# Performance work log

Hardware: AMD Instinct MI355X
Metric: run time of the kernel (lower is better)

The kernel has to match this reference:

```python
import jax, jax.numpy as jnp
import numpy as np
import math

D_MODEL = 1024
NUM_HEADS = 16
HEAD_DIM = D_MODEL // NUM_HEADS  # 64
PLANE_DIM = HEAD_DIM // 2        # 32
ROPE_THETA = 10000.0
ROPE_PERIOD = 1024.0
ROPE_SCALE = 2.0 * math.pi / ROPE_PERIOD


def _inv_freq():
    # 1 / theta^(arange(0, plane_dim, 2)/plane_dim)  -> [plane_dim//2] = [16]
    return 1.0 / ROPE_THETA ** (jnp.arange(0, PLANE_DIM, 2, dtype=jnp.float32) / PLANE_DIM)


def _rotate_pairs(x, sin, cos):
    # x: [B,H,N,P], sin/cos: [B,1,N,P//2]
    x0 = x[..., 0::2]
    x1 = x[..., 1::2]
    y0 = x0 * cos - x1 * sin
    y1 = x0 * sin + x1 * cos
    return jnp.stack([y0, y1], axis=-1).reshape(x.shape)


def _apply_rope_2d(x, pos_2d, inv_freq):
    # x: [B,H,N,D], pos_2d: [B,N,2]
    ang_x = pos_2d[..., 0] * ROPE_SCALE  # [B,N]
    ang_y = pos_2d[..., 1] * ROPE_SCALE
    fx = ang_x[..., None] * inv_freq     # [B,N,P//2]
    fy = ang_y[..., None] * inv_freq
    sin_x, cos_x = jnp.sin(fx)[:, None], jnp.cos(fx)[:, None]  # [B,1,N,P//2]
    sin_y, cos_y = jnp.sin(fy)[:, None], jnp.cos(fy)[:, None]
    xp, yp = x[..., :PLANE_DIM], x[..., PLANE_DIM:]
    xp = _rotate_pairs(xp, sin_x, cos_x)
    yp = _rotate_pairs(yp, sin_y, cos_y)
    return jnp.concatenate([xp, yp], axis=-1)


def setup_inputs() -> dict:
    key = jax.random.key(0)
    ks = jax.random.split(key, 12)
    B, N, d = 2, 2048, D_MODEL
    s = 1.0 / math.sqrt(d)
    return {
        "x": jax.random.normal(ks[0], (B, N, d), jnp.float32),
        "q_positions": jax.random.uniform(ks[1], (B, N, 2), jnp.float32) * ROPE_PERIOD,
        "kv_positions": jax.random.uniform(ks[2], (B, N, 2), jnp.float32) * ROPE_PERIOD,
        "Wq": jax.random.normal(ks[3], (d, d), jnp.float32) * s,
        "bq": jnp.zeros((d,), jnp.float32),
        "Wk": jax.random.normal(ks[4], (d, d), jnp.float32) * s,
        "bk": jnp.zeros((d,), jnp.float32),
        "Wv": jax.random.normal(ks[5], (d, d), jnp.float32) * s,
        "bv": jnp.zeros((d,), jnp.float32),
        "Wo": jax.random.normal(ks[6], (d, d), jnp.float32) * s,
        "bo": jnp.zeros((d,), jnp.float32),
    }


def reference(x, q_positions, kv_positions, Wq, bq, Wk, bk, Wv, bv, Wo, bo):
    B, Nq, _ = x.shape
    H, D = NUM_HEADS, HEAD_DIM
    inv_freq = _inv_freq()
    # fused-style QKV projections (torch Linear: x @ W.T + b)
    q = (jnp.einsum('bnd,od->bno', x, Wq) + bq).reshape(B, Nq, H, D).transpose(0, 2, 1, 3)
    k = (jnp.einsum('bnd,od->bno', x, Wk) + bk).reshape(B, Nq, H, D).transpose(0, 2, 1, 3)
    v = (jnp.einsum('bnd,od->bno', x, Wv) + bv).reshape(B, Nq, H, D).transpose(0, 2, 1, 3)
    q = _apply_rope_2d(q, q_positions, inv_freq)
    k = _apply_rope_2d(k, kv_positions, inv_freq)
    logits = jnp.einsum('bhqd,bhkd->bhqk', q, k) / math.sqrt(D)
    attn = jax.nn.softmax(logits, axis=-1)
    out = jnp.einsum('bhqk,bhkd->bhqd', attn, v)
    out = out.transpose(0, 2, 1, 3).reshape(B, Nq, D_MODEL)
    return jnp.einsum('bnd,od->bno', out, Wo) + bo
```

## Files before the change

### kernel.cpp

```cpp
#include <hip/hip_runtime.h>
#include <math.h>

#define SEQ   2048
#define DM    1024
#define NTOK  4096
#define HEADS 16
#define HDIM  64
#define ROPE_SCALE 0.006135923151542565f

#define TM 64
#define TN 64
#define TK 32

typedef __attribute__((ext_vector_type(8))) short bf16x8;
typedef __attribute__((ext_vector_type(4))) float f32x4;

__device__ __forceinline__ unsigned short f2bf(float f) {
    unsigned int u = __float_as_uint(f);
    return (unsigned short)((u + 0x7FFFu + ((u >> 16) & 1u)) >> 16);
}
__device__ __forceinline__ float bf2f(unsigned short h) {
    return __uint_as_float(((unsigned int)h) << 16);
}

__global__ __launch_bounds__(256) void qkv_rope(
    const float* __restrict__ x,
    const float* __restrict__ Wq, const float* __restrict__ bq,
    const float* __restrict__ Wk, const float* __restrict__ bk,
    const float* __restrict__ Wv, const float* __restrict__ bv,
    const float* __restrict__ qpos, const float* __restrict__ kpos,
    float* __restrict__ qo, float* __restrict__ ko, float* __restrict__ vo)
{
    const int proj = blockIdx.z;
    const float* W   = proj==0 ? Wq : (proj==1 ? Wk : Wv);
    const float* bia = proj==0 ? bq : (proj==1 ? bk : bv);
    float* out       = proj==0 ? qo : (proj==1 ? ko : vo);
    const float* pos = proj==0 ? qpos : kpos;

    __shared__ __align__(16) float As[TK][TM+4];
    __shared__ __align__(16) float Bs[TK][TN+4];

    const int tx = threadIdx.x, ty = threadIdx.y;
    const int tid = ty*16 + tx;
    const int m0 = blockIdx.y * TM;
    const int n0 = blockIdx.x * TN;

    float acc[4][4] = {};

    for (int k0 = 0; k0 < DM; k0 += TK) {
        for (int f = tid; f < 512; f += 256) {
            const int r = f >> 3, c4 = (f & 7) * 4;
            float4 a = *(const float4*)(x + (size_t)(m0 + r)*DM + k0 + c4);
            As[c4+0][r]=a.x; As[c4+1][r]=a.y; As[c4+2][r]=a.z; As[c4+3][r]=a.w;
            float4 b = *(const float4*)(W + (size_t)(n0 + r)*DM + k0 + c4);
            Bs[c4+0][r]=b.x; Bs[c4+1][r]=b.y; Bs[c4+2][r]=b.z; Bs[c4+3][r]=b.w;
        }
        __syncthreads();
        #pragma unroll
        for (int kk = 0; kk < TK; ++kk) {
            float4 a4 = *(const float4*)&As[kk][ty*4];
            float4 b4 = *(const float4*)&Bs[kk][tx*4];
            const float av[4] = {a4.x,a4.y,a4.z,a4.w};
            const float bv4[4] = {b4.x,b4.y,b4.z,b4.w};
            #pragma unroll
            for (int i=0;i<4;++i)
                #pragma unroll
                for (int j=0;j<4;++j)
                    acc[i][j] += av[i]*bv4[j];
        }
        __syncthreads();
    }

    #pragma unroll
    for (int i=0;i<4;++i) {
        const int tok = m0 + ty*4 + i;
        const int b   = tok >> 11;
        const int n   = tok & (SEQ-1);
        if (proj == 2) {
            #pragma unroll
            for (int j=0;j<4;++j) {
                const int o = n0 + tx*4 + j;
                const int h = o >> 6, dd = o & 63;
                out[(((size_t)(b*HEADS + h))*SEQ + n)*HDIM + dd] = acc[i][j] + bia[o];
            }
        } else {
            #pragma unroll
            for (int j=0;j<4;j+=2) {
                const int o = n0 + tx*4 + j;
                const int h = o >> 6, dd = o & 63;
                const int plane = (dd < 32) ? 0 : 1;
                const float p = pos[((size_t)(b*SEQ + n))*2 + plane];
                const float e = (float)(dd & 31) * (1.0f/32.0f);
                const float invf = 1.0f / powf(10000.0f, e);
                const float ang = p * ROPE_SCALE * invf;
                float s, c;
                sincosf(ang, &s, &c);
                const float a0 = acc[i][j]   + bia[o];
                const float a1 = acc[i][j+1] + bia[o+1];
                const size_t base = (((size_t)(b*HEADS + h))*SEQ + n)*HDIM + dd;
                out[base]   = a0*c - a1*s;
                out[base+1] = a0*s + a1*c;
            }
        }
    }
}

#define KB 32

__global__ __launch_bounds__(256) void attn_mfma(
    const float* __restrict__ q, const float* __restrict__ k,
    const float* __restrict__ v, float* __restrict__ ao)
{
    const int bh  = blockIdx.y;
    const int qb0 = blockIdx.x * 128;
    const int tid = threadIdx.x;
    const int lane = tid & 63;
    const int wv   = tid >> 6;
    const int col  = lane & 15;
    const int grp  = lane >> 4;

    __shared__ __align__(16) unsigned short Khi[KB][72];
    __shared__ __align__(16) unsigned short Klo[KB][72];
    __shared__ __align__(16) unsigned short Vthi[HDIM][40];
    __shared__ __align__(16) unsigned short Vtlo[HDIM][40];
    __shared__ __align__(16) unsigned short Pb[4][32][40];

    const float* kbase = k + (size_t)bh*SEQ*HDIM;
    const float* vbase = v + (size_t)bh*SEQ*HDIM;

    bf16x8 qhi[2][2], qlo[2][2];
    #pragma unroll
    for (int mf = 0; mf < 2; ++mf)
        #pragma unroll
        for (int ks = 0; ks < 2; ++ks) {
            const float* p = q + ((size_t)bh*SEQ + qb0 + wv*32 + mf*16 + col)*HDIM
                               + ks*32 + grp*8;
            float4 f0 = ((const float4*)p)[0];
            float4 f1 = ((const float4*)p)[1];
            float fv[8] = {f0.x,f0.y,f0.z,f0.w,f1.x,f1.y,f1.z,f1.w};
            bf16x8 h, l;
            #pragma unroll
            for (int j = 0; j < 8; ++j) {
                unsigned short hb = f2bf(fv[j]);
                h[j] = (short)hb;
                l[j] = (short)f2bf(fv[j] - bf2f(hb));
            }
            qhi[mf][ks] = h; qlo[mf][ks] = l;
        }

    f32x4 o[2][4];
    #pragma unroll
    for (int mf=0; mf<2; ++mf)
        #pragma unroll
        for (int nf=0; nf<4; ++nf)
            o[mf][nf] = (f32x4)0.f;
    float mrun[2][4], lrun[2][4];
    #pragma unroll
    for (int mf=0; mf<2; ++mf)
        #pragma unroll
        for (int r=0; r<4; ++r) { mrun[mf][r] = -INFINITY; lrun[mf][r] = 0.f; }

    for (int kt = 0; kt < SEQ; kt += KB) {
        __syncthreads();
        {
            const int row = tid >> 3, c0 = (tid & 7) * 8;
            const float* src = kbase + (size_t)(kt + row)*HDIM + c0;
            float4 f0 = ((const float4*)src)[0];
            float4 f1 = ((const float4*)src)[1];
            float fv[8] = {f0.x,f0.y,f0.z,f0.w,f1.x,f1.y,f1.z,f1.w};
            bf16x8 h, l;
            #pragma unroll
            for (int j = 0; j < 8; ++j) {
                unsigned short hb = f2bf(fv[j]);
                h[j] = (short)hb;
                l[j] = (short)f2bf(fv[j] - bf2f(hb));
            }
            *(bf16x8*)&Khi[row][c0] = h;
            *(bf16x8*)&Klo[row][c0] = l;
        }
        {
            const int key = tid & 31, db = tid >> 5;
            const float* src = vbase + (size_t)(kt + key)*HDIM + db*8;
            float4 f0 = ((const float4*)src)[0];
            float4 f1 = ((const float4*)src)[1];
            float fv[8] = {f0.x,f0.y,f0.z,f0.w,f1.x,f1.y,f1.z,f1.w};
            #pragma unroll
            for (int j = 0; j < 8; ++j) {
                unsigned short hb = f2bf(fv[j]);
                Vthi[db*8+j][key] = hb;
                Vtlo[db*8+j][key] = f2bf(fv[j] - bf2f(hb));
            }
        }
        __syncthreads();

        f32x4 s[2][2];
        #pragma unroll
        for (int mf=0; mf<2; ++mf)
            #pragma unroll
            for (int nf=0; nf<2; ++nf)
                s[mf][nf] = (f32x4)0.f;
        #pragma unroll
        for (int ks = 0; ks < 2; ++ks) {
            bf16x8 kh[2], kl[2];
            #pragma unroll
            for (int nf = 0; nf < 2; ++nf) {
                kh[nf] = *(const bf16x8*)&Khi[nf*16 + col][ks*32 + grp*8];
                kl[nf] = *(const bf16x8*)&Klo[nf*16 + col][ks*32 + grp*8];
            }
            #pragma unroll
            for (int mf = 0; mf < 2; ++mf)
                #pragma unroll
                for (int nf = 0; nf < 2; ++nf) {
                    s[mf][nf] = __builtin_amdgcn_mfma_f32_16x16x32_bf16(qhi[mf][ks], kh[nf], s[mf][nf], 0,0,0);
                    s[mf][nf] = __builtin_amdgcn_mfma_f32_16x16x32_bf16(qlo[mf][ks], kh[nf], s[mf][nf], 0,0,0);
                    s[mf][nf] = __builtin_amdgcn_mfma_f32_16x16x32_bf16(qhi[mf][ks], kl[nf], s[mf][nf], 0,0,0);
                }
        }

        #pragma unroll
        for (int mf=0; mf<2; ++mf)
            #pragma unroll
            for (int nf=0; nf<2; ++nf)
                s[mf][nf] *= 0.125f;

        #pragma unroll
        for (int mf = 0; mf < 2; ++mf) {
            #pragma unroll
            for (int r = 0; r < 4; ++r) {
                float m2 = fmaxf(s[mf][0][r], s[mf][1][r]);
                m2 = fmaxf(m2, __shfl_xor(m2, 1, 16));
                m2 = fmaxf(m2, __shfl_xor(m2, 2, 16));
                m2 = fmaxf(m2, __shfl_xor(m2, 4, 16));
                m2 = fmaxf(m2, __shfl_xor(m2, 8, 16));
                const float mnew = fmaxf(mrun[mf][r], m2);
                const float corr = __expf(mrun[mf][r] - mnew);
                mrun[mf][r] = mnew;
                const float p0 = __expf(s[mf][0][r] - mnew);
                const float p1 = __expf(s[mf][1][r] - mnew);
                float ts = p0 + p1;
                ts += __shfl_xor(ts, 1, 16);
                ts += __shfl_xor(ts, 2, 16);
                ts += __shfl_xor(ts, 4, 16);
                ts += __shfl_xor(ts, 8, 16);
                lrun[mf][r] = lrun[mf][r]*corr + ts;
                #pragma unroll
                for (int nf=0; nf<4; ++nf) o[mf][nf][r] *= corr;
                Pb[wv][mf*16 + grp*4 + r][col]      = f2bf(p0);
                Pb[wv][mf*16 + grp*4 + r][16 + col] = f2bf(p1);
            }
        }

        bf16x8 pa[2];
        #pragma unroll
        for (int mf=0; mf<2; ++mf)
            pa[mf] = *(const bf16x8*)&Pb[wv][mf*16 + col][grp*8];
        #pragma unroll
        for (int nf = 0; nf < 4; ++nf) {
            bf16x8 vh = *(const bf16x8*)&Vthi[nf*16 + col][grp*8];
            bf16x8 vl = *(const bf16x8*)&Vtlo[nf*16 + col][grp*8];
            #pragma unroll
            for (int mf = 0; mf < 2; ++mf) {
                o[mf][nf] = __builtin_amdgcn_mfma_f32_16x16x32_bf16(pa[mf], vh, o[mf][nf], 0,0,0);
                o[mf][nf] = __builtin_amdgcn_mfma_f32_16x16x32_bf16(pa[mf], vl, o[mf][nf], 0,0,0);
            }
        }
    }

    const int b = bh >> 4, h = bh & 15;
    #pragma unroll
    for (int mf = 0; mf < 2; ++mf)
        #pragma unroll
        for (int r = 0; r < 4; ++r) {
            const float inv = 1.0f / lrun[mf][r];
            const int n = qb0 + wv*32 + mf*16 + grp*4 + r;
            float* orow = ao + (((size_t)b*SEQ + n)*HEADS + h)*HDIM;
            #pragma unroll
            for (int nf = 0; nf < 4; ++nf)
                orow[nf*16 + col] = o[mf][nf][r] * inv;
        }
}

__global__ __launch_bounds__(256) void out_proj(
    const float* __restrict__ ao, const float* __restrict__ Wo,
    const float* __restrict__ bo, float* __restrict__ out)
{
    __shared__ __align__(16) float As[TK][TM+4];
    __shared__ __align__(16) float Bs[TK][TN+4];

    const int tx = threadIdx.x, ty = threadIdx.y;
    const int tid = ty*16 + tx;
    const int m0 = blockIdx.y * TM;
    const int n0 = blockIdx.x * TN;

    float acc[4][4] = {};

    for (int k0 = 0; k0 < DM; k0 += TK) {
        for (int f = tid; f < 512; f += 256) {
            const int r = f >> 3, c4 = (f & 7) * 4;
            float4 a = *(const float4*)(ao + (size_t)(m0 + r)*DM + k0 + c4);
            As[c4+0][r]=a.x; As[c4+1][r]=a.y; As[c4+2][r]=a.z; As[c4+3][r]=a.w;
            float4 b = *(const float4*)(Wo + (size_t)(n0 + r)*DM + k0 + c4);
            Bs[c4+0][r]=b.x; Bs[c4+1][r]=b.y; Bs[c4+2][r]=b.z; Bs[c4+3][r]=b.w;
        }
        __syncthreads();
        #pragma unroll
        for (int kk = 0; kk < TK; ++kk) {
            float4 a4 = *(const float4*)&As[kk][ty*4];
            float4 b4 = *(const float4*)&Bs[kk][tx*4];
            const float av[4] = {a4.x,a4.y,a4.z,a4.w};
            const float bv4[4] = {b4.x,b4.y,b4.z,b4.w};
            #pragma unroll
            for (int i=0;i<4;++i)
                #pragma unroll
                for (int j=0;j<4;++j)
                    acc[i][j] += av[i]*bv4[j];
        }
        __syncthreads();
    }

    #pragma unroll
    for (int i=0;i<4;++i) {
        const int tok = m0 + ty*4 + i;
        #pragma unroll
        for (int j=0;j<4;++j) {
            const int o = n0 + tx*4 + j;
            out[(size_t)tok*DM + o] = acc[i][j] + bo[o];
        }
    }
}

extern "C" void kernel_launch(void* const* d_in, const int* in_sizes, int n_in,
                              void* d_out, int out_size, void* d_ws, size_t ws_size,
                              hipStream_t stream)
{
    const float* x    = (const float*)d_in[0];
    const float* qpos = (const float*)d_in[1];
    const float* kpos = (const float*)d_in[2];
    const float* Wq   = (const float*)d_in[3];
    const float* bq   = (const float*)d_in[4];
    const float* Wk   = (const float*)d_in[5];
    const float* bk   = (const float*)d_in[6];
    const float* Wv   = (const float*)d_in[7];
    const float* bv   = (const float*)d_in[8];
    const float* Wo   = (const float*)d_in[9];
    const float* bo   = (const float*)d_in[10];
    float* out = (float*)d_out;

    float* qw = (float*)d_ws;
    float* kw = qw + (size_t)NTOK*DM;
    float* vw = kw + (size_t)NTOK*DM;
    float* aw = vw + (size_t)NTOK*DM;

    dim3 blk(16,16);
    qkv_rope<<<dim3(DM/TN, NTOK/TM, 3), blk, 0, stream>>>(
        x, Wq,bq, Wk,bk, Wv,bv, qpos,kpos, qw,kw,vw);
    attn_mfma<<<dim3(SEQ/128, 2*HEADS), 256, 0, stream>>>(qw, kw, vw, aw);
    out_proj<<<dim3(DM/TN, NTOK/TM), blk, 0, stream>>>(aw, Wo, bo, out);
}
```

Baseline: 753.2 us.

## Replace FP32 SIMT projection GEMMs with split-bf16 MFMA GEMM using packed swizzled tiles

Result: faster. 657.5 us (-12.7%).

```diff
diff --git a/kernel.cpp b/kernel.cpp
--- a/kernel.cpp
+++ b/kernel.cpp
@@ -7,10 +7,7 @@
 #define HEADS 16
 #define HDIM  64
 #define ROPE_SCALE 0.006135923151542565f
-
-#define TM 64
-#define TN 64
-#define TK 32
+#define L2_10000   13.287712379549449f
 
 typedef __attribute__((ext_vector_type(8))) short bf16x8;
 typedef __attribute__((ext_vector_type(4))) float f32x4;
@@ -23,83 +20,184 @@
     return __uint_as_float(((unsigned int)h) << 16);
 }
 
-__global__ __launch_bounds__(256) void qkv_rope(
-    const float* __restrict__ x,
-    const float* __restrict__ Wq, const float* __restrict__ bq,
-    const float* __restrict__ Wk, const float* __restrict__ bk,
-    const float* __restrict__ Wv, const float* __restrict__ bv,
+__device__ __forceinline__ void split8(const float* __restrict__ src, bf16x8& h, bf16x8& l) {
+    float4 f0 = ((const float4*)src)[0];
+    float4 f1 = ((const float4*)src)[1];
+    float fv[8] = {f0.x,f0.y,f0.z,f0.w,f1.x,f1.y,f1.z,f1.w};
+    #pragma unroll
+    for (int j = 0; j < 8; ++j) {
+        unsigned short hb = f2bf(fv[j]);
+        h[j] = (short)hb;
+        l[j] = (short)f2bf(fv[j] - bf2f(hb));
+    }
+}
+
+__device__ __forceinline__ void gload16(const void* g, void* l) {
+    __builtin_amdgcn_global_load_lds(
+        (const __attribute__((address_space(1))) unsigned int*)g,
+        (__attribute__((address_space(3))) unsigned int*)l, 16, 0, 0);
+}
+
+__global__ __launch_bounds__(256) void pack_swz(
+    const float* __restrict__ src, unsigned short* __restrict__ dst)
+{
+    const int idx = blockIdx.x*256 + threadIdx.x;
+    const int e = idx * 8;
+    const int r = e >> 10, k0 = e & 1023;
+    bf16x8 h, l;
+    split8(src + (size_t)r*DM + k0, h, l);
+    const int mt = r >> 7, rl = r & 127;
+    const int kt = k0 >> 5, kl = k0 & 31;
+    char* tb = (char*)(dst + ((size_t)(mt*32 + kt))*8192);
+    const int sw = (rl & 7) << 4;
+    *(bf16x8*)(tb + ((rl*128 + kl*2) ^ sw))      = h;
+    *(bf16x8*)(tb + ((rl*128 + 64 + kl*2) ^ sw)) = l;
+}
+
+__global__ __launch_bounds__(256) void pack_swz3(
+    const float* __restrict__ Wq, const float* __restrict__ Wk,
+    const float* __restrict__ Wv, unsigned short* __restrict__ dst)
+{
+    const int idx = blockIdx.x*256 + threadIdx.x;
+    const int e = idx * 8;
+    const int r = e >> 10, k0 = e & 1023;
+    const int proj = r >> 10;
+    const float* W = proj==0 ? Wq : (proj==1 ? Wk : Wv);
+    bf16x8 h, l;
+    split8(W + (size_t)(r & 1023)*DM + k0, h, l);
+    const int mt = r >> 7, rl = r & 127;
+    const int kt = k0 >> 5, kl = k0 & 31;
+    char* tb = (char*)(dst + ((size_t)(mt*32 + kt))*8192);
+    const int sw = (rl & 7) << 4;
+    *(bf16x8*)(tb + ((rl*128 + kl*2) ^ sw))      = h;
+    *(bf16x8*)(tb + ((rl*128 + 64 + kl*2) ^ sw)) = l;
+}
+
+__global__ __launch_bounds__(256) void gemm_mfma(
+    const unsigned short* __restrict__ Ap, const unsigned short* __restrict__ Bp,
+    const int mode,
+    const float* __restrict__ bq, const float* __restrict__ bk,
+    const float* __restrict__ bv,
     const float* __restrict__ qpos, const float* __restrict__ kpos,
-    float* __restrict__ qo, float* __restrict__ ko, float* __restrict__ vo)
+    float* __restrict__ qo, float* __restrict__ ko, float* __restrict__ vo,
+    const float* __restrict__ bo, float* __restrict__ outp)
 {
-    const int proj = blockIdx.z;
-    const float* W   = proj==0 ? Wq : (proj==1 ? Wk : Wv);
-    const float* bia = proj==0 ? bq : (proj==1 ? bk : bv);
-    float* out       = proj==0 ? qo : (proj==1 ? ko : vo);
-    const float* pos = proj==0 ? qpos : kpos;
-
-    __shared__ __align__(16) float As[TK][TM+4];
-    __shared__ __align__(16) float Bs[TK][TN+4];
-
-    const int tx = threadIdx.x, ty = threadIdx.y;
-    const int tid = ty*16 + tx;
-    const int m0 = blockIdx.y * TM;
-    const int n0 = blockIdx.x * TN;
-
-    float acc[4][4] = {};
-
-    for (int k0 = 0; k0 < DM; k0 += TK) {
-        for (int f = tid; f < 512; f += 256) {
-            const int r = f >> 3, c4 = (f & 7) * 4;
-            float4 a = *(const float4*)(x + (size_t)(m0 + r)*DM + k0 + c4);
-            As[c4+0][r]=a.x; As[c4+1][r]=a.y; As[c4+2][r]=a.z; As[c4+3][r]=a.w;
-            float4 b = *(const float4*)(W + (size_t)(n0 + r)*DM + k0 + c4);
-            Bs[c4+0][r]=b.x; Bs[c4+1][r]=b.y; Bs[c4+2][r]=b.z; Bs[c4+3][r]=b.w;
-        }
+    __shared__ __align__(16) unsigned short Ab[2][8192];
+    __shared__ __align__(16) unsigned short Bb[2][8192];
+
+    const int tid = threadIdx.x, lane = tid & 63, wv = tid >> 6;
+    const int col = lane & 15, grp = lane >> 4;
+    const int wr = wv >> 1, wc = wv & 1;
+    const int mt = blockIdx.y, nt = blockIdx.x;
+
+    f32x4 acc[4][4];
+    #pragma unroll
+    for (int mf=0; mf<4; ++mf)
+        #pragma unroll
+        for (int nf=0; nf<4; ++nf)
+            acc[mf][nf] = (f32x4)0.f;
+
+    auto stage = [&](int buf, int kt) {
+        const char* ga = (const char*)(Ap + ((size_t)(mt*32 + kt))*8192);
+        const char* gb = (const char*)(Bp + ((size_t)(nt*32 + kt))*8192);
+        char* la = (char*)&Ab[buf][0];
+        char* lb = (char*)&Bb[buf][0];
+        #pragma unroll
+        for (int rep = 0; rep < 4; ++rep) {
+            const int o = wv*4096 + rep*1024;
+            gload16(ga + o + lane*16, la + o);
+            gload16(gb + o + lane*16, lb + o);
+        }
+    };
+
+    stage(0, 0);
+    int cur = 0;
+    for (int kt = 0; kt < 32; ++kt) {
         __syncthreads();
-        #pragma unroll
-        for (int kk = 0; kk < TK; ++kk) {
-            float4 a4 = *(const float4*)&As[kk][ty*4];
-            float4 b4 = *(const float4*)&Bs[kk][tx*4];
-            const float av[4] = {a4.x,a4.y,a4.z,a4.w};
-            const float bv4[4] = {b4.x,b4.y,b4.z,b4.w};
-            #pragma unroll
-            for (int i=0;i<4;++i)
+        if (kt < 31) stage(cur ^ 1, kt + 1);
+        const char* A = (const char*)&Ab[cur][0];
+        const char* B = (const char*)&Bb[cur][0];
+        bf16x8 ah[4], al[4], bh[4], bl[4];
+        #pragma unroll
+        for (int mf = 0; mf < 4; ++mf) {
+            const int rl = wr*64 + mf*16 + col;
+            const int base = rl*128 + grp*16;
+            const int sw = (rl & 7) << 4;
+            ah[mf] = *(const bf16x8*)(A + (base ^ sw));
+            al[mf] = *(const bf16x8*)(A + ((base + 64) ^ sw));
+        }
+        #pragma unroll
+        for (int nf = 0; nf < 4; ++nf) {
+            const int rl = wc*64 + nf*16 + col;
+            const int base = rl*128 + grp*16;
+            const int sw = (rl & 7) << 4;
+            bh[nf] = *(const bf16x8*)(B + (base ^ sw));
+            bl[nf] = *(const bf16x8*)(B + ((base + 64) ^ sw));
+        }
+        #pragma unroll
+        for (int mf = 0; mf < 4; ++mf)
+            #pragma unroll
+            for (int nf = 0; nf < 4; ++nf) {
+                acc[mf][nf] = __builtin_amdgcn_mfma_f32_16x16x32_bf16(ah[mf], bh[nf], acc[mf][nf], 0,0,0);
+                acc[mf][nf] = __builtin_amdgcn_mfma_f32_16x16x32_bf16(ah[mf], bl[nf], acc[mf][nf], 0,0,0);
+                acc[mf][nf] = __builtin_amdgcn_mfma_f32_16x16x32_bf16(al[mf], bh[nf], acc[mf][nf], 0,0,0);
+            }
+        cur ^= 1;
+    }
+
+    const int m0 = mt*128, n0 = nt*128;
+    if (mode == 1) {
+        #pragma unroll
+        for (int nf = 0; nf < 4; ++nf) {
+            const int n = n0 + wc*64 + nf*16 + col;
+            const float bn = bo[n];
+            #pragma unroll
+            for (int mf = 0; mf < 4; ++mf)
                 #pragma unroll
-                for (int j=0;j<4;++j)
-                    acc[i][j] += av[i]*bv4[j];
-        }
-        __syncthreads();
-    }
-
-    #pragma unroll
-    for (int i=0;i<4;++i) {
-        const int tok = m0 + ty*4 + i;
-        const int b   = tok >> 11;
-        const int n   = tok & (SEQ-1);
-        if (proj == 2) {
-            #pragma unroll
-            for (int j=0;j<4;++j) {
-                const int o = n0 + tx*4 + j;
-                const int h = o >> 6, dd = o & 63;
-                out[(((size_t)(b*HEADS + h))*SEQ + n)*HDIM + dd] = acc[i][j] + bia[o];
-            }
-        } else {
-            #pragma unroll
-            for (int j=0;j<4;j+=2) {
-                const int o = n0 + tx*4 + j;
-                const int h = o >> 6, dd = o & 63;
-                const int plane = (dd < 32) ? 0 : 1;
-                const float p = pos[((size_t)(b*SEQ + n))*2 + plane];
-                const float e = (float)(dd & 31) * (1.0f/32.0f);
-                const float invf = 1.0f / powf(10000.0f, e);
-                const float ang = p * ROPE_SCALE * invf;
-                float s, c;
-                sincosf(ang, &s, &c);
-                const float a0 = acc[i][j]   + bia[o];
-                const float a1 = acc[i][j+1] + bia[o+1];
-                const size_t base = (((size_t)(b*HEADS + h))*SEQ + n)*HDIM + dd;
-                out[base]   = a0*c - a1*s;
-                out[base+1] = a0*s + a1*c;
+                for (int i = 0; i < 4; ++i) {
+                    const int tok = m0 + wr*64 + mf*16 + grp*4 + i;
+                    outp[(size_t)tok*DM + n] = acc[mf][nf][i] + bn;
+                }
+        }
+    } else {
+        const int proj = n0 >> 10;
+        const float* bb = proj==0 ? bq : (proj==1 ? bk : bv);
+        float* op       = proj==0 ? qo : (proj==1 ? ko : vo);
+        const float* pp = proj==0 ? qpos : kpos;
+        #pragma unroll
+        for (int nf = 0; nf < 4; ++nf) {
+            const int n  = n0 + wc*64 + nf*16 + col;
+            const int nn = n & 1023;
+            const int h  = nn >> 6, dd = nn & 63;
+            const float bn = bb[nn];
+            if (proj == 2) {
+                #pragma unroll
+                for (int mf = 0; mf < 4; ++mf)
+                    #pragma unroll
+                    for (int i = 0; i < 4; ++i) {
+                        const int tok = m0 + wr*64 + mf*16 + grp*4 + i;
+                        const int b = tok >> 11, sq = tok & 2047;
+                        op[(((size_t)(b*HEADS + h))*SEQ + sq)*HDIM + dd] = acc[mf][nf][i] + bn;
+                    }
+            } else {
+                const int plane = dd >> 5;
+                const float e = (float)(dd & 30) * (1.0f/32.0f);
+                const float invf = exp2f(-L2_10000 * e);
+                #pragma unroll
+                for (int mf = 0; mf < 4; ++mf)
+                    #pragma unroll
+                    for (int i = 0; i < 4; ++i) {
+                        const int tok = m0 + wr*64 + mf*16 + grp*4 + i;
+                        const int b = tok >> 11, sq = tok & 2047;
+                        const float pv = pp[((size_t)(b*SEQ + sq))*2 + plane];
+                        const float ang = pv * ROPE_SCALE * invf;
+                        float s, c;
+                        sincosf(ang, &s, &c);
+                        const float val = acc[mf][nf][i] + bn;
+                        const float prt = __shfl_xor(val, 1);
+                        const float res = (dd & 1) ? (prt*s + val*c) : (val*c - prt*s);
+                        op[(((size_t)(b*HEADS + h))*SEQ + sq)*HDIM + dd] = res;
+                    }
             }
         }
     }
@@ -135,17 +233,7 @@
         for (int ks = 0; ks < 2; ++ks) {
             const float* p = q + ((size_t)bh*SEQ + qb0 + wv*32 + mf*16 + col)*HDIM
                                + ks*32 + grp*8;
-            float4 f0 = ((const float4*)p)[0];
-            float4 f1 = ((const float4*)p)[1];
-            float fv[8] = {f0.x,f0.y,f0.z,f0.w,f1.x,f1.y,f1.z,f1.w};
-            bf16x8 h, l;
-            #pragma unroll
-            for (int j = 0; j < 8; ++j) {
-                unsigned short hb = f2bf(fv[j]);
-                h[j] = (short)hb;
-                l[j] = (short)f2bf(fv[j] - bf2f(hb));
-            }
-            qhi[mf][ks] = h; qlo[mf][ks] = l;
+            split8(p, qhi[mf][ks], qlo[mf][ks]);
         }
 
     f32x4 o[2][4];
@@ -164,17 +252,8 @@
         __syncthreads();
         {
             const int row = tid >> 3, c0 = (tid & 7) * 8;
-            const float* src = kbase + (size_t)(kt + row)*HDIM + c0;
-            float4 f0 = ((const float4*)src)[0];
-            float4 f1 = ((const float4*)src)[1];
-            float fv[8] = {f0.x,f0.y,f0.z,f0.w,f1.x,f1.y,f1.z,f1.w};
             bf16x8 h, l;
-            #pragma unroll
-            for (int j = 0; j < 8; ++j) {
-                unsigned short hb = f2bf(fv[j]);
-                h[j] = (short)hb;
-                l[j] = (short)f2bf(fv[j] - bf2f(hb));
-            }
+            split8(kbase + (size_t)(kt + row)*HDIM + c0, h, l);
             *(bf16x8*)&Khi[row][c0] = h;
             *(bf16x8*)&Klo[row][c0] = l;
         }
@@ -280,55 +359,6 @@
         }
 }
 
-__global__ __launch_bounds__(256) void out_proj(
-    const float* __restrict__ ao, const float* __restrict__ Wo,
-    const float* __restrict__ bo, float* __restrict__ out)
-{
-    __shared__ __align__(16) float As[TK][TM+4];
-    __shared__ __align__(16) float Bs[TK][TN+4];
-
-    const int tx = threadIdx.x, ty = threadIdx.y;
-    const int tid = ty*16 + tx;
-    const int m0 = blockIdx.y * TM;
-    const int n0 = blockIdx.x * TN;
-
-    float acc[4][4] = {};
-
-    for (int k0 = 0; k0 < DM; k0 += TK) {
-        for (int f = tid; f < 512; f += 256) {
-            const int r = f >> 3, c4 = (f & 7) * 4;
-            float4 a = *(const float4*)(ao + (size_t)(m0 + r)*DM + k0 + c4);
-            As[c4+0][r]=a.x; As[c4+1][r]=a.y; As[c4+2][r]=a.z; As[c4+3][r]=a.w;
-            float4 b = *(const float4*)(Wo + (size_t)(n0 + r)*DM + k0 + c4);
-            Bs[c4+0][r]=b.x; Bs[c4+1][r]=b.y; Bs[c4+2][r]=b.z; Bs[c4+3][r]=b.w;
-        }
-        __syncthreads();
-        #pragma unroll
-        for (int kk = 0; kk < TK; ++kk) {
-            float4 a4 = *(const float4*)&As[kk][ty*4];
-            float4 b4 = *(const float4*)&Bs[kk][tx*4];
-            const float av[4] = {a4.x,a4.y,a4.z,a4.w};
-            const float bv4[4] = {b4.x,b4.y,b4.z,b4.w};
-            #pragma unroll
-            for (int i=0;i<4;++i)
-                #pragma unroll
-                for (int j=0;j<4;++j)
-                    acc[i][j] += av[i]*bv4[j];
-        }
-        __syncthreads();
-    }
-
-    #pragma unroll
-    for (int i=0;i<4;++i) {
-        const int tok = m0 + ty*4 + i;
-        #pragma unroll
-        for (int j=0;j<4;++j) {
-            const int o = n0 + tx*4 + j;
-            out[(size_t)tok*DM + o] = acc[i][j] + bo[o];
-        }
-    }
-}
-
 extern "C" void kernel_launch(void* const* d_in, const int* in_sizes, int n_in,
                               void* d_out, int out_size, void* d_ws, size_t ws_size,
                               hipStream_t stream)
@@ -349,11 +379,22 @@
     float* qw = (float*)d_ws;
     float* kw = qw + (size_t)NTOK*DM;
     float* vw = kw + (size_t)NTOK*DM;
-    float* aw = vw + (size_t)NTOK*DM;
-
-    dim3 blk(16,16);
-    qkv_rope<<<dim3(DM/TN, NTOK/TM, 3), blk, 0, stream>>>(
-        x, Wq,bq, Wk,bk, Wv,bv, qpos,kpos, qw,kw,vw);
-    attn_mfma<<<dim3(SEQ/128, 2*HEADS), 256, 0, stream>>>(qw, kw, vw, aw);
-    out_proj<<<dim3(DM/TN, NTOK/TM), blk, 0, stream>>>(aw, Wo, bo, out);
-}
+    unsigned short* Xp    = (unsigned short*)(vw + (size_t)NTOK*DM);
+    unsigned short* Wqkvp = Xp + (size_t)NTOK*DM*2;
+    unsigned short* Wop   = Wqkvp + (size_t)3*DM*DM*2;
+
+    pack_swz <<<2048, 256, 0, stream>>>(x, Xp);
+    pack_swz3<<<1536, 256, 0, stream>>>(Wq, Wk, Wv, Wqkvp);
+    pack_swz <<< 512, 256, 0, stream>>>(Wo, Wop);
+
+    gemm_mfma<<<dim3(24, 32), 256, 0, stream>>>(
+        Xp, Wqkvp, 0, bq, bk, bv, qpos, kpos, qw, kw, vw, nullptr, nullptr);
+
+    attn_mfma<<<dim3(SEQ/128, 2*HEADS), 256, 0, stream>>>(qw, kw, vw, out);
+
+    pack_swz <<<2048, 256, 0, stream>>>(out, Xp);
+
+    gemm_mfma<<<dim3(8, 32), 256, 0, stream>>>(
+        Xp, Wop, 1, nullptr, nullptr, nullptr, nullptr, nullptr,
+        nullptr, nullptr, nullptr, bo, out);
+}
```
